# Performance work log

Hardware: AMD Instinct MI355X
Metric: run time of the kernel (lower is better)

## Reference

```python
import jax, jax.numpy as jnp
import numpy as np
from jax import lax

N, T, E = 20000, 64, 640000
H, OUT, HEADS = 128, 64, 3
NEG_SLOPE = 0.2  # GATConv default negative_slope


def setup_inputs() -> dict:
    key = jax.random.key(0)
    ks = jax.random.split(key, 10)
    s = 0.1
    return {
        "node_features": jax.random.normal(ks[0], (N, T), jnp.float32),
        "edge_index": jax.random.randint(ks[1], (2, E), 0, N, dtype=jnp.int32),
        "edge_attributes": jax.random.uniform(ks[2], (E,), jnp.float32),
        "lstm_Wih": jax.random.normal(ks[3], (4 * H, 1), jnp.float32) * s,
        "lstm_Whh": jax.random.normal(ks[4], (4 * H, H), jnp.float32) * s,
        "lstm_bih": jnp.zeros((4 * H,), jnp.float32),
        "lstm_bhh": jnp.zeros((4 * H,), jnp.float32),
        "gcn_W": jax.random.normal(ks[5], (H, H), jnp.float32) * s,
        "gcn_b": jnp.zeros((H,), jnp.float32),
        "gat_W": jax.random.normal(ks[6], (HEADS * OUT, H), jnp.float32) * s,
        "gat_att_src": jax.random.normal(ks[7], (HEADS, OUT), jnp.float32) * s,
        "gat_att_dst": jax.random.normal(ks[8], (HEADS, OUT), jnp.float32) * s,
        "gat_b": jnp.zeros((HEADS * OUT,), jnp.float32),
    }


def _lstm_last(x, Wih, Whh, bih, bhh):
    """x: [N, T, 1] -> last hidden state [N, H] (torch gate order i,f,g,o)."""
    n = x.shape[0]
    h_dim = Whh.shape[1]
    b = bih + bhh

    def step(carry, xt):
        h, c = carry
        g = xt @ Wih.T + h @ Whh.T + b  # [N, 4H]
        i, f, gg, o = jnp.split(g, 4, axis=-1)
        c = jax.nn.sigmoid(f) * c + jax.nn.sigmoid(i) * jnp.tanh(gg)
        h = jax.nn.sigmoid(o) * jnp.tanh(c)
        return (h, c), None

    init = (jnp.zeros((n, h_dim), x.dtype), jnp.zeros((n, h_dim), x.dtype))
    (h, _), _ = lax.scan(step, init, jnp.swapaxes(x, 0, 1))
    return h


def _add_self_loops(row, col, n):
    loop = jnp.arange(n, dtype=row.dtype)
    return jnp.concatenate([row, loop]), jnp.concatenate([col, loop])


def _gcn(x, row, col, edge_weight, W, b):
    """PyG GCNConv: self-loops (weight 1), symmetric normalization, W x + b."""
    n = x.shape[0]
    row, col = _add_self_loops(row, col, n)
    ew = jnp.concatenate([edge_weight, jnp.ones((n,), edge_weight.dtype)])
    x = x @ W.T  # [N, H]
    deg = jax.ops.segment_sum(ew, col, num_segments=n)
    dinv = jnp.where(deg > 0, deg ** -0.5, 0.0)
    norm = dinv[row] * ew * dinv[col]  # [E+N]
    out = jax.ops.segment_sum(x[row] * norm[:, None], col, num_segments=n)
    return out + b


def _gat(x, row, col, W, att_src, att_dst, b):
    """PyG GATConv (concat=True): self-loops, edge softmax over incoming edges."""
    n = x.shape[0]
    heads, c = att_src.shape
    xh = (x @ W.T).reshape(n, heads, c)  # [N, Hd, C]
    a_src = jnp.einsum('nhc,hc->nh', xh, att_src)  # [N, Hd]
    a_dst = jnp.einsum('nhc,hc->nh', xh, att_dst)
    row, col = _add_self_loops(row, col, n)
    alpha = jax.nn.leaky_relu(a_src[row] + a_dst[col], NEG_SLOPE)  # [E', Hd]
    amax = jax.ops.segment_max(alpha, col, num_segments=n)
    alpha = jnp.exp(alpha - amax[col])
    denom = jax.ops.segment_sum(alpha, col, num_segments=n)
    alpha = alpha / denom[col]
    out = jax.ops.segment_sum(xh[row] * alpha[:, :, None], col, num_segments=n)
    return out.reshape(n, heads * c) + b


def reference(node_features, edge_index, edge_attributes,
              lstm_Wih, lstm_Whh, lstm_bih, lstm_bhh,
              gcn_W, gcn_b, gat_W, gat_att_src, gat_att_dst, gat_b):
    x = node_features[:, :, None]  # [N, T, 1]
    x = _lstm_last(x, lstm_Wih, lstm_Whh, lstm_bih, lstm_bhh)  # [N, H]
    x = jax.nn.relu(x)
    row, col = edge_index[0], edge_index[1]
    x = _gcn(x, row, col, edge_attributes, gcn_W, gcn_b)
    x = jax.nn.relu(x)
    x = _gat(x, row, col, gat_W, gat_att_src, gat_att_dst, gat_b)  # [N, Hd*C]
    return jnp.mean(x, axis=0, keepdims=True)  # global_mean_pool, batch=None -> [1, Hd*C]
```

## Files before the change

### kernel.cpp

```cpp
#include <hip/hip_runtime.h>


#define N_NODES 20000
#define T_STEPS 64
#define N_EDGES 640000
#define HDIM    128
#define JOUT    192
#define NEG_SLOPE 0.2f
#define EDGE_CAP 128
#define NBW     16
#define NGRP    5
#define NBB     (NBW * NGRP)
#define BTHR    640
#define NBLK    250
#define GRIDX   256
#define LDS_W     131072
#define LDS_BW    4096
#define LDS_SCR   (NGRP * 4096)
#define LDS_FLG   256
#define LDS_TOTAL (LDS_W + LDS_BW + LDS_SCR + LDS_FLG)

#define L2E  1.4426950408889634f
#define K2E  2.8853900817779268f

typedef _Float16 half8 __attribute__((ext_vector_type(8)));
typedef _Float16 half4v __attribute__((ext_vector_type(4)));
typedef _Float16 half2v __attribute__((ext_vector_type(2)));
typedef float floatx4 __attribute__((ext_vector_type(4)));

__device__ __forceinline__ float lrelu(float x) { return x > 0.f ? x : NEG_SLOPE * x; }

__global__ void pack_whh_kernel(const float* __restrict__ Whh,
                                _Float16* __restrict__ Wpack)
{
  int i = blockIdx.x * 256 + threadIdx.x;
  int tile = i >> 6, lane = i & 63;
  int nt = tile >> 2, kt = tile & 3;
  int row = nt * 16 + (lane & 15);
  int c0  = kt * 32 + (lane >> 4) * 8;
  const float sc = ((row >> 7) == 2) ? K2E : L2E;
  half8 v;
  #pragma unroll
  for (int j = 0; j < 8; ++j)
    v[j] = (_Float16)(Whh[row * 128 + c0 + j] * sc);
  *(half8*)&Wpack[(size_t)i * 8] = v;
}

template <int M>
__global__ void pack_w_kernel(const float* __restrict__ W,
                              _Float16* __restrict__ P)
{
  int i = blockIdx.x * 256 + threadIdx.x;
  int tile = i >> 6, lane = i & 63;
  int mt = tile >> 2, kt = tile & 3;
  int row = mt * 16 + (lane & 15);
  int c0  = kt * 32 + (lane >> 4) * 8;
  half8 v;
  #pragma unroll
  for (int j = 0; j < 8; ++j)
    v[j] = (_Float16)W[row * 128 + c0 + j];
  *(half8*)&P[(size_t)i * 8] = v;
}


#define INITACC(L, acc) do {                                                  \
  _Pragma("unroll") for (int g_ = 0; g_ < 4; ++g_) {                          \
    const float4 p0_ = *(const float4*)&bwRole[g_ * 128 + (L) * 16];          \
    const float4 p1_ = *(const float4*)&bwRole[g_ * 128 + (L) * 16 + 2];      \
    acc[g_][0] = p0_.x + xv * p0_.y;                                          \
    acc[g_][1] = p0_.z + xv * p0_.w;                                          \
    acc[g_][2] = p1_.x + xv * p1_.y;                                          \
    acc[g_][3] = p1_.z + xv * p1_.w;                                          \
  }                                                                           \
} while (0)

#define LDA(buf, L, KT) do {                                                  \
  _Pragma("unroll") for (int g_ = 0; g_ < 4; ++g_)                            \
    buf[g_] = *(const half8*)&WlRole[g_ * 16384 + (L) * 2048 + (KT) * 512];   \
} while (0)

#define MFA(acc, buf, KT) do {                                                \
  _Pragma("unroll") for (int g_ = 0; g_ < 4; ++g_)                            \
    acc[g_] = __builtin_amdgcn_mfma_f32_16x16x32_f16(                         \
        buf[g_], Bf[(KT)], acc[g_], 0, 0, 0);                                 \
} while (0)

#define PHASE4(L, acc) do {                                                   \
  const int cg_ = cgb + (L);                                                  \
  half4v hpack;                                                               \
  _Pragma("unroll") for (int r_ = 0; r_ < 4; ++r_) {                          \
    const float Be = __builtin_amdgcn_exp2f(-acc[0][r_]);                     \
    const float Ae = __builtin_amdgcn_exp2f(-acc[1][r_]);                     \
    const float De = __builtin_amdgcn_exp2f(acc[2][r_]);                      \
    const float Ee = __builtin_amdgcn_exp2f(-acc[3][r_]);                     \
    const float Ap = Ae + 1.f;                                                \
    const float Bp = Be + 1.f;                                                \
    const float Dp = De + 1.f;                                                \
    const float Nn = cst[(L) * 4 + r_] * Bp * Dp + Ap * (De - 1.f);           \
    const float cv = Nn * __builtin_amdgcn_rcpf(Ap * Bp * Dp);                \
    cst[(L) * 4 + r_] = cv;                                                   \
    const float cvc = fminf(fmaxf(cv, -10.f), 10.f);                          \
    const float Fe = __builtin_amdgcn_exp2f(K2E * cvc);                       \
    hpack[r_] = (_Float16)((Fe - 1.f) *                                       \
                __builtin_amdgcn_rcpf((Ee + 1.f) * (Fe + 1.f)));              \
  }                                                                           \
  const int lp_ = nl + 16 * (2 * (cg_ & 1) + wq_hi);                          \
  *(half4v*)&myscr[(cg_ >> 1) * 512 + lp_ * 8 + j0] = hpack;                  \
} while (0)

#define SB __builtin_amdgcn_sched_barrier(0)

#define SIGNAL(arr, val) do {                                                 \
  __threadfence_block();                                                      \
  if (ln == 0) arr[wv] = (val);                                               \
} while (0)
#define WAITGE(arr, val) do {                                                 \
  if (ln == 0) { while (arr[pw] < (val)) __builtin_amdgcn_s_sleep(1); }       \
  __builtin_amdgcn_wave_barrier();                                            \
  __threadfence_block();                                                      \
} while (0)

#define LSTM_STEP(t) do {                                                     \
  WAITGE(flW, (t));                                                           \
  half8 Bf[4];                                                                \
  _Pragma("unroll") for (int kt_ = 0; kt_ < 4; ++kt_)                         \
    Bf[kt_] = *(const half8*)&scrLane[kt_ * 512];                             \
  SIGNAL(flR, (t) + 1);                                                       \
  floatx4 accA[4], accB[4];                                                   \
  half8 Aa[4], Ab[4];                                                         \
                                                                  \
  INITACC(0, accA);                                                           \
  LDA(Aa, 0, 0); LDA(Ab, 0, 1);                                               \
  MFA(accA, Aa, 0); LDA(Aa, 0, 2);                                            \
  MFA(accA, Ab, 1); LDA(Ab, 0, 3);                                            \
  MFA(accA, Aa, 2); MFA(accA, Ab, 3);                                         \
                                                                  \
  INITACC(1, accB); LDA(Aa, 1, 0); LDA(Ab, 1, 1);                             \
  WAITGE(flR, (t) + 1);                                                       \
  SB; PHASE4(0, accA);                                                        \
  MFA(accB, Aa, 0); LDA(Aa, 1, 2);                                            \
  MFA(accB, Ab, 1); LDA(Ab, 1, 3);                                            \
  MFA(accB, Aa, 2); MFA(accB, Ab, 3);                                         \
                                                                  \
  INITACC(2, accA); LDA(Aa, 2, 0); LDA(Ab, 2, 1);                             \
  SB; PHASE4(1, accB);                                                        \
  MFA(accA, Aa, 0); LDA(Aa, 2, 2);                                            \
  MFA(accA, Ab, 1); LDA(Ab, 2, 3);                                            \
  MFA(accA, Aa, 2); MFA(accA, Ab, 3);                                         \
                                                                  \
  INITACC(3, accB); LDA(Aa, 3, 0); LDA(Ab, 3, 1);                             \
  SB; PHASE4(2, accA);                                                        \
  MFA(accB, Aa, 0); LDA(Aa, 3, 2);                                            \
  MFA(accB, Ab, 1); LDA(Ab, 3, 3);                                            \
  MFA(accB, Aa, 2); MFA(accB, Ab, 3);                                         \
  PHASE4(3, accB);                                                            \
  SIGNAL(flW, (t) + 1);                                                       \
} while (0)

__global__ __attribute__((amdgpu_flat_work_group_size(BTHR, BTHR),
                          amdgpu_waves_per_eu(3, 3)))
void lstm_stream_kernel(
    const float* __restrict__ xfeat, const _Float16* __restrict__ Wpack,
    const float* __restrict__ Wih, const float* __restrict__ bih,
    const float* __restrict__ bhh, _Float16* __restrict__ x1,
    const int* __restrict__ ei, const float* __restrict__ ew,
    int* __restrict__ cnt, int2* __restrict__ pairB)
{
  const int tid  = threadIdx.x;

  if (blockIdx.x >= NBLK) {
    const int stride = (GRIDX - NBLK) * BTHR;
    for (int e = (blockIdx.x - NBLK) * BTHR + tid; e < N_EDGES; e += stride) {
      const int r = ei[e];
      const int c = ei[N_EDGES + e];
      const float w = ew[e];
      const int p = atomicAdd(&cnt[c], 1);
      pairB[(size_t)c * EDGE_CAP + p] = make_int2(r, __float_as_int(w));
    }
    return;
  }

  extern __shared__ char dynlds[];
  _Float16* Wl  = (_Float16*)dynlds;
  float2*   bw  = (float2*)(dynlds + LDS_W);
  _Float16* scr = (_Float16*)(dynlds + LDS_W + LDS_BW);
  volatile int* flR = (volatile int*)(dynlds + LDS_W + LDS_BW + LDS_SCR);
  volatile int* flW = flR + 16;

  const int wv   = tid >> 6;
  const int pw   = wv ^ 1;
  const int grp  = wv >> 1;
  const int role = wv & 1;
  const int cgb  = role * 4;
  const int ln   = tid & 63;
  const int nl   = ln & 15;
  const int quad = ln >> 4;
  const int n0   = blockIdx.x * NBB + grp * NBW;

  {
    const float4* src = (const float4*)Wpack;
    float4* dst = (float4*)Wl;
    for (int i = tid; i < LDS_W / 16; i += BTHR) dst[i] = src[i];
  }
  for (int i = tid; i < 512; i += BTHR) {
    const float sc = ((i >> 7) == 2) ? K2E : L2E;
    bw[i] = make_float2((bih[i] + bhh[i]) * sc, Wih[i] * sc);
  }
  {
    float4* z = (float4*)scr;
    for (int i = tid; i < LDS_SCR / 16; i += BTHR)
      z[i] = make_float4(0.f, 0.f, 0.f, 0.f);
  }
  if (tid < 32) { flR[tid] = 0; flW[tid] = 0; }
  __syncthreads();

  _Float16* myscr = scr + grp * 2048;
  const _Float16* WlRole  = Wl + (size_t)cgb * 2048 + (size_t)ln * 8;
  const float2*   bwRole  = bw + cgb * 16 + quad * 4;
  const _Float16* scrLane = myscr + (size_t)ln * 8;
  const float* xrow = xfeat + (size_t)(n0 + nl) * T_STEPS;

  float cst[16];
  #pragma unroll
  for (int i = 0; i < 16; ++i) cst[i] = 0.f;

  const int wq_hi = quad >> 1;
  const int j0    = (quad & 1) * 4;

  float xv = xrow[0];

  #pragma unroll 1
  for (int t = 0; t < T_STEPS; ++t) {
    const float xn = xrow[(t + 1 <= 63) ? (t + 1) : 63];
    LSTM_STEP(t);
    xv = xn;
  }

  #pragma unroll
  for (int k = 0; k < 2; ++k) {
    const int kt = role * 2 + k;
    half8 hf = *(const half8*)&scrLane[kt * 512];
    #pragma unroll
    for (int j = 0; j < 8; ++j)
      hf[j] = (_Float16)fmaxf((float)hf[j], 0.f);
    *(half8*)&x1[(size_t)(n0 + nl) * HDIM + kt * 32 + quad * 8] = hf;
  }
}

template <int J>
__global__ __launch_bounds__(320) void gemm_mfma(
    const _Float16* __restrict__ X, const _Float16* __restrict__ P,
    _Float16* __restrict__ Y)
{
  const int ln = threadIdx.x & 63;
  const int wv = threadIdx.x >> 6;
  const int node = blockIdx.x * 80 + wv * 16 + (ln & 15);
  const int ko = (ln >> 4) * 8;
  half8 Bf[4];
  #pragma unroll
  for (int kt = 0; kt < 4; ++kt)
    Bf[kt] = *(const half8*)&X[(size_t)node * 128 + kt * 32 + ko];
  #pragma unroll
  for (int m = 0; m < J / 16; ++m) {
    floatx4 acc = {0.f, 0.f, 0.f, 0.f};
    #pragma unroll
    for (int kt = 0; kt < 4; ++kt) {
      const half8 Af = *(const half8*)&P[(size_t)((m * 4 + kt) * 64 + ln) * 8];
      acc = __builtin_amdgcn_mfma_f32_16x16x32_f16(Af, Bf[kt], acc, 0, 0, 0);
    }
    half4v o;
    #pragma unroll
    for (int j = 0; j < 4; ++j) o[j] = (_Float16)acc[j];
    *(half4v*)&Y[(size_t)node * J + m * 16 + (ln >> 4) * 4] = o;
  }
}

__global__ __launch_bounds__(320) void gemm_mfma_att(
    const _Float16* __restrict__ X, const _Float16* __restrict__ P,
    const float* __restrict__ att_src, const float* __restrict__ att_dst,
    _Float16* __restrict__ Y, float4* __restrict__ asrc,
    float4* __restrict__ adst)
{
  __shared__ float aS[JOUT], aD[JOUT];
  const int tid = threadIdx.x;
  for (int i = tid; i < JOUT; i += 320) { aS[i] = att_src[i]; aD[i] = att_dst[i]; }
  __syncthreads();
  const int ln = tid & 63;
  const int wv = tid >> 6;
  const int quad = ln >> 4;
  const int node = blockIdx.x * 80 + wv * 16 + (ln & 15);
  half8 Bf[4];
  #pragma unroll
  for (int kt = 0; kt < 4; ++kt)
    Bf[kt] = *(const half8*)&X[(size_t)node * 128 + kt * 32 + quad * 8];
  float sA[3] = {0.f, 0.f, 0.f}, sD[3] = {0.f, 0.f, 0.f};
  #pragma unroll
  for (int m = 0; m < JOUT / 16; ++m) {
    floatx4 acc = {0.f, 0.f, 0.f, 0.f};
    #pragma unroll
    for (int kt = 0; kt < 4; ++kt) {
      const half8 Af = *(const half8*)&P[(size_t)((m * 4 + kt) * 64 + ln) * 8];
      acc = __builtin_amdgcn_mfma_f32_16x16x32_f16(Af, Bf[kt], acc, 0, 0, 0);
    }
    const int h  = m >> 2;
    const int jo = (m & 3) * 16 + quad * 4;
    half4v o;
    #pragma unroll
    for (int j = 0; j < 4; ++j) {
      sA[h] += acc[j] * aS[h * 64 + jo + j];
      sD[h] += acc[j] * aD[h * 64 + jo + j];
      o[j] = (_Float16)acc[j];
    }
    *(half4v*)&Y[(size_t)node * JOUT + m * 16 + quad * 4] = o;
  }
  #pragma unroll
  for (int h = 0; h < 3; ++h) {
    sA[h] += __shfl_xor(sA[h], 16); sA[h] += __shfl_xor(sA[h], 32);
    sD[h] += __shfl_xor(sD[h], 16); sD[h] += __shfl_xor(sD[h], 32);
  }
  if (quad == 0) {
    asrc[node] = make_float4(sA[0], sA[1], sA[2], 0.f);
    adst[node] = make_float4(sD[0], sD[1], sD[2], 0.f);
  }
}

__global__ void zero_kernel(int* __restrict__ cnt, float* __restrict__ accum)
{
  int i = blockIdx.x * 256 + threadIdx.x;
  if (i < N_NODES) cnt[i] = 0;
  if (i < JOUT) accum[i] = 0.f;
}

__global__ __launch_bounds__(256) void degdinv_kernel(
    const int* __restrict__ cnt, const int2* __restrict__ pairB,
    float* __restrict__ dinv)
{
  const int lane = threadIdx.x & 63;
  const int wv = threadIdx.x >> 6;
  const int c = blockIdx.x * 4 + wv;
  const int cc = cnt[c];
  const size_t base = (size_t)c * EDGE_CAP;
  float s = 0.f;
  for (int k = lane; k < cc; k += 64)
    s += __int_as_float(pairB[base + k].y);
  #pragma unroll
  for (int off = 1; off < 64; off <<= 1) s += __shfl_xor(s, off);
  if (lane == 0) dinv[c] = rsqrtf(s + 1.0f);
}

__global__ __launch_bounds__(256) void gcn_agg_kernel(
    const _Float16* __restrict__ y, const float* __restrict__ dinv,
    const int* __restrict__ cnt, const int2* __restrict__ pairB,
    const float* __restrict__ gcn_b, _Float16* __restrict__ x2)
{
  __shared__ float2 stg[4][64];
  const int lane = threadIdx.x & 63;
  const int wv = threadIdx.x >> 6;
  const int c = blockIdx.x * 4 + wv;
  const float dc = dinv[c];
  const half2v* y2 = (const half2v*)y;
  half2v yc = y2[c * 64 + lane];
  float ax = (float)yc[0] * dc * dc, ay = (float)yc[1] * dc * dc;
  const int cc = cnt[c];
  const size_t base = (size_t)c * EDGE_CAP;
  for (int tb = 0; tb < cc; tb += 64) {
    const int nedge = min(64, cc - tb);
    const int k = tb + lane;
    if (k < cc) {
      const int2 pr = pairB[base + k];
      stg[wv][lane] = make_float2(__int_as_float(pr.x),
                                  __int_as_float(pr.y) * dinv[pr.x] * dc);
    }
    __builtin_amdgcn_wave_barrier();
    int i = 0;
    for (; i + 4 <= nedge; i += 4) {
      float2 p0 = stg[wv][i],     p1 = stg[wv][i + 1];
      float2 p2 = stg[wv][i + 2], p3 = stg[wv][i + 3];
      const half2v a0 = y2[(size_t)__float_as_int(p0.x) * 64 + lane];
      const half2v a1 = y2[(size_t)__float_as_int(p1.x) * 64 + lane];
      const half2v a2 = y2[(size_t)__float_as_int(p2.x) * 64 + lane];
      const half2v a3 = y2[(size_t)__float_as_int(p3.x) * 64 + lane];
      ax += (float)a0[0] * p0.y + (float)a1[0] * p1.y +
            (float)a2[0] * p2.y + (float)a3[0] * p3.y;
      ay += (float)a0[1] * p0.y + (float)a1[1] * p1.y +
            (float)a2[1] * p2.y + (float)a3[1] * p3.y;
    }
    for (; i < nedge; ++i) {
      float2 p0 = stg[wv][i];
      const half2v a0 = y2[(size_t)__float_as_int(p0.x) * 64 + lane];
      ax += (float)a0[0] * p0.y; ay += (float)a0[1] * p0.y;
    }
    __builtin_amdgcn_wave_barrier();
  }
  int j0 = lane * 2;
  half2v o;
  o[0] = (_Float16)fmaxf(ax + gcn_b[j0], 0.f);
  o[1] = (_Float16)fmaxf(ay + gcn_b[j0 + 1], 0.f);
  *(half2v*)&x2[c * 128 + j0] = o;
}

__global__ __launch_bounds__(256) void gat_agg_kernel(
    const _Float16* __restrict__ xh, const float4* __restrict__ asrc,
    const float4* __restrict__ adst, const int* __restrict__ cnt,
    const int2* __restrict__ pairB, float* __restrict__ accum)
{
  __shared__ float4 cstg[4][64];
  const int lane = threadIdx.x & 63;
  const int wv = threadIdx.x >> 6;
  const int c = blockIdx.x * 4 + wv;
  const int cc = cnt[c];
  const size_t base = (size_t)c * EDGE_CAP;
  float4 adc = adst[c];
  float4 asc = asrc[c];
  const float se0 = __expf(lrelu(asc.x + adc.x));
  const float se1 = __expf(lrelu(asc.y + adc.y));
  const float se2 = __expf(lrelu(asc.z + adc.z));

  float o0 = se0 * (float)xh[c * JOUT + lane];
  float o1 = se1 * (float)xh[c * JOUT + 64 + lane];
  float o2 = se2 * (float)xh[c * JOUT + 128 + lane];
  float dp0 = 0.f, dp1 = 0.f, dp2 = 0.f;

  for (int tb = 0; tb < cc; tb += 64) {
    const int nedge = min(64, cc - tb);
    const int k = tb + lane;
    if (k < cc) {
      const int s = pairB[base + k].x;
      const float4 av = asrc[s];
      const float a0 = __expf(lrelu(av.x + adc.x));
      const float a1 = __expf(lrelu(av.y + adc.y));
      const float a2 = __expf(lrelu(av.z + adc.z));
      dp0 += a0; dp1 += a1; dp2 += a2;
      cstg[wv][lane] = make_float4(__int_as_float(s), a0, a1, a2);
    }
    __builtin_amdgcn_wave_barrier();
    int i = 0;
    for (; i + 2 <= nedge; i += 2) {
      float4 q0 = cstg[wv][i], q1 = cstg[wv][i + 1];
      const _Float16* r0 = xh + (size_t)__float_as_int(q0.x) * JOUT;
      const _Float16* r1 = xh + (size_t)__float_as_int(q1.x) * JOUT;
      float a0 = (float)r0[lane], b0 = (float)r0[64 + lane], g0 = (float)r0[128 + lane];
      float a1 = (float)r1[lane], b1 = (float)r1[64 + lane], g1 = (float)r1[128 + lane];
      o0 += q0.y * a0 + q1.y * a1;
      o1 += q0.z * b0 + q1.z * b1;
      o2 += q0.w * g0 + q1.w * g1;
    }
    for (; i < nedge; ++i) {
      float4 q0 = cstg[wv][i];
      const _Float16* r0 = xh + (size_t)__float_as_int(q0.x) * JOUT;
      o0 += q0.y * (float)r0[lane];
      o1 += q0.z * (float)r0[64 + lane];
      o2 += q0.w * (float)r0[128 + lane];
    }
    __builtin_amdgcn_wave_barrier();
  }

  #pragma unroll
  for (int off = 1; off < 64; off <<= 1) {
    dp0 += __shfl_xor(dp0, off);
    dp1 += __shfl_xor(dp1, off);
    dp2 += __shfl_xor(dp2, off);
  }
  const float iv0 = 1.f / (dp0 + se0);
  const float iv1 = 1.f / (dp1 + se1);
  const float iv2 = 1.f / (dp2 + se2);
  o0 *= iv0; o1 *= iv1; o2 *= iv2;

  __shared__ float red[4][JOUT];
  red[wv][lane]       = o0;
  red[wv][64 + lane]  = o1;
  red[wv][128 + lane] = o2;
  __syncthreads();
  if (threadIdx.x < JOUT) {
    float sum = red[0][threadIdx.x] + red[1][threadIdx.x] +
                red[2][threadIdx.x] + red[3][threadIdx.x];
    atomicAdd(&accum[threadIdx.x], sum);
  }
}

__global__ void finalize_kernel(const float* __restrict__ accum,
                                const float* __restrict__ gat_b,
                                float* __restrict__ out)
{
  int j = threadIdx.x;
  if (j < JOUT) out[j] = accum[j] * (1.0f / N_NODES) + gat_b[j];
}

extern "C" void kernel_launch(void* const* d_in, const int* in_sizes, int n_in,
                              void* d_out, int out_size, void* d_ws, size_t ws_size,
                              hipStream_t stream)
{
  const float* xfeat = (const float*)d_in[0];
  const int*   eidx  = (const int*)d_in[1];
  const float* eattr = (const float*)d_in[2];
  const float* Wih   = (const float*)d_in[3];
  const float* Whh   = (const float*)d_in[4];
  const float* bihp  = (const float*)d_in[5];
  const float* bhhp  = (const float*)d_in[6];
  const float* gcnW  = (const float*)d_in[7];
  const float* gcnb  = (const float*)d_in[8];
  const float* gatW  = (const float*)d_in[9];
  const float* attS  = (const float*)d_in[10];
  const float* attD  = (const float*)d_in[11];
  const float* gatb  = (const float*)d_in[12];
  float* out = (float*)d_out;

  char* ws = (char*)d_ws;
  size_t off = 0;
  auto alloc = [&](size_t bytes) {
    char* p = ws + off;
    off += (bytes + 255) & ~size_t(255);
    return p;
  };
  _Float16*  x1     = (_Float16*)alloc((size_t)N_NODES * 128 * 2);
  _Float16*  y      = (_Float16*)alloc((size_t)N_NODES * 128 * 2);
  _Float16*  x2     = (_Float16*)alloc((size_t)N_NODES * 128 * 2);
  _Float16*  xh     = (_Float16*)alloc((size_t)N_NODES * 192 * 2);
  float4*    asrc   = (float4*)alloc((size_t)N_NODES * 16);
  float4*    adst   = (float4*)alloc((size_t)N_NODES * 16);
  float*     dinv   = (float*)alloc((size_t)N_NODES * 4);
  int*       cnt    = (int*)alloc((size_t)N_NODES * 4);
  int2*      pairB  = (int2*)alloc((size_t)N_NODES * EDGE_CAP * 8);
  float*     accum  = (float*)alloc(JOUT * 4);
  _Float16*  wpack  = (_Float16*)alloc(131072);
  _Float16*  wpackG = (_Float16*)alloc((size_t)128 * 128 * 2);
  _Float16*  wpackA = (_Float16*)alloc((size_t)192 * 128 * 2);

  hipFuncSetAttribute((const void*)lstm_stream_kernel,
                      hipFuncAttributeMaxDynamicSharedMemorySize, LDS_TOTAL);

  zero_kernel<<<(N_NODES + 255) / 256, 256, 0, stream>>>(cnt, accum);
  pack_whh_kernel<<<32, 256, 0, stream>>>(Whh, wpack);
  pack_w_kernel<128><<<8, 256, 0, stream>>>(gcnW, wpackG);
  pack_w_kernel<192><<<12, 256, 0, stream>>>(gatW, wpackA);
  lstm_stream_kernel<<<GRIDX, BTHR, LDS_TOTAL, stream>>>(
      xfeat, wpack, Wih, bihp, bhhp, x1, eidx, eattr, cnt, pairB);
  degdinv_kernel<<<N_NODES / 4, 256, 0, stream>>>(cnt, pairB, dinv);
  gemm_mfma<128><<<N_NODES / 80, 320, 0, stream>>>(x1, wpackG, y);
  gcn_agg_kernel<<<N_NODES / 4, 256, 0, stream>>>(y, dinv, cnt, pairB, gcnb, x2);
  gemm_mfma_att<<<N_NODES / 80, 320, 0, stream>>>(x2, wpackA, attS, attD,
                                                  xh, asrc, adst);
  gat_agg_kernel<<<N_NODES / 4, 256, 0, stream>>>(xh, asrc, adst, cnt, pairB, accum);
  finalize_kernel<<<1, 256, 0, stream>>>(accum, gatb, out);
}
```

Measured before the change: 594.2 us.

## Reorder GAT mean-pool to sum per-source attention weights, fuse prep kernels

```diff
diff --git a/kernel.cpp b/kernel.cpp
--- a/kernel.cpp
+++ b/kernel.cpp
@@ -30,36 +30,54 @@
 
 __device__ __forceinline__ float lrelu(float x) { return x > 0.f ? x : NEG_SLOPE * x; }
 
-__global__ void pack_whh_kernel(const float* __restrict__ Whh,
-                                _Float16* __restrict__ Wpack)
-{
-  int i = blockIdx.x * 256 + threadIdx.x;
-  int tile = i >> 6, lane = i & 63;
-  int nt = tile >> 2, kt = tile & 3;
-  int row = nt * 16 + (lane & 15);
-  int c0  = kt * 32 + (lane >> 4) * 8;
-  const float sc = ((row >> 7) == 2) ? K2E : L2E;
-  half8 v;
-  #pragma unroll
-  for (int j = 0; j < 8; ++j)
-    v[j] = (_Float16)(Whh[row * 128 + c0 + j] * sc);
-  *(half8*)&Wpack[(size_t)i * 8] = v;
-}
-
-template <int M>
-__global__ void pack_w_kernel(const float* __restrict__ W,
-                              _Float16* __restrict__ P)
-{
-  int i = blockIdx.x * 256 + threadIdx.x;
-  int tile = i >> 6, lane = i & 63;
-  int mt = tile >> 2, kt = tile & 3;
-  int row = mt * 16 + (lane & 15);
-  int c0  = kt * 32 + (lane >> 4) * 8;
-  half8 v;
-  #pragma unroll
-  for (int j = 0; j < 8; ++j)
-    v[j] = (_Float16)W[row * 128 + c0 + j];
-  *(half8*)&P[(size_t)i * 8] = v;
+__global__ __launch_bounds__(256) void prep_kernel(
+    const float* __restrict__ Whh, _Float16* __restrict__ Wpack,
+    const float* __restrict__ gcnW, _Float16* __restrict__ WpackG,
+    const float* __restrict__ gatW, _Float16* __restrict__ WpackA,
+    int* __restrict__ cnt, float* __restrict__ Wgt, float* __restrict__ accum)
+{
+  const int b = blockIdx.x;
+  const int tid = threadIdx.x;
+  if (b < 32) {
+    int i = b * 256 + tid;
+    int tile = i >> 6, lane = i & 63;
+    int nt = tile >> 2, kt = tile & 3;
+    int row = nt * 16 + (lane & 15);
+    int c0  = kt * 32 + (lane >> 4) * 8;
+    const float sc = ((row >> 7) == 2) ? K2E : L2E;
+    half8 v;
+    #pragma unroll
+    for (int j = 0; j < 8; ++j)
+      v[j] = (_Float16)(Whh[row * 128 + c0 + j] * sc);
+    *(half8*)&Wpack[(size_t)i * 8] = v;
+  } else if (b < 40) {
+    int i = (b - 32) * 256 + tid;
+    int tile = i >> 6, lane = i & 63;
+    int mt = tile >> 2, kt = tile & 3;
+    int row = mt * 16 + (lane & 15);
+    int c0  = kt * 32 + (lane >> 4) * 8;
+    half8 v;
+    #pragma unroll
+    for (int j = 0; j < 8; ++j) v[j] = (_Float16)gcnW[row * 128 + c0 + j];
+    *(half8*)&WpackG[(size_t)i * 8] = v;
+  } else if (b < 52) {
+    int i = (b - 40) * 256 + tid;
+    int tile = i >> 6, lane = i & 63;
+    int mt = tile >> 2, kt = tile & 3;
+    int row = mt * 16 + (lane & 15);
+    int c0  = kt * 32 + (lane >> 4) * 8;
+    half8 v;
+    #pragma unroll
+    for (int j = 0; j < 8; ++j) v[j] = (_Float16)gatW[row * 128 + c0 + j];
+    *(half8*)&WpackA[(size_t)i * 8] = v;
+  } else {
+    int i = (b - 52) * 256 + tid;
+    if (i < N_NODES) {
+      cnt[i] = 0;
+      *(float4*)&Wgt[i * 4] = make_float4(0.f, 0.f, 0.f, 0.f);
+    }
+    if (i < JOUT) accum[i] = 0.f;
+  }
 }
 
 
@@ -247,13 +265,25 @@
   }
 }
 
-template <int J>
-__global__ __launch_bounds__(320) void gemm_mfma(
+__global__ __launch_bounds__(320) void gemm128_deg_kernel(
     const _Float16* __restrict__ X, const _Float16* __restrict__ P,
-    _Float16* __restrict__ Y)
+    _Float16* __restrict__ Y, const int* __restrict__ cnt,
+    const int2* __restrict__ pairB, float* __restrict__ dinv)
 {
   const int ln = threadIdx.x & 63;
   const int wv = threadIdx.x >> 6;
+  if (blockIdx.x >= 250) {
+    const int c = (blockIdx.x - 250) * 5 + wv;
+    const int cc = cnt[c];
+    const size_t base = (size_t)c * EDGE_CAP;
+    float s = 0.f;
+    for (int k = ln; k < cc; k += 64)
+      s += __int_as_float(pairB[base + k].y);
+    #pragma unroll
+    for (int off = 1; off < 64; off <<= 1) s += __shfl_xor(s, off);
+    if (ln == 0) dinv[c] = rsqrtf(s + 1.0f);
+    return;
+  }
   const int node = blockIdx.x * 80 + wv * 16 + (ln & 15);
   const int ko = (ln >> 4) * 8;
   half8 Bf[4];
@@ -261,7 +291,7 @@
   for (int kt = 0; kt < 4; ++kt)
     Bf[kt] = *(const half8*)&X[(size_t)node * 128 + kt * 32 + ko];
   #pragma unroll
-  for (int m = 0; m < J / 16; ++m) {
+  for (int m = 0; m < 8; ++m) {
     floatx4 acc = {0.f, 0.f, 0.f, 0.f};
     #pragma unroll
     for (int kt = 0; kt < 4; ++kt) {
@@ -271,7 +301,7 @@
     half4v o;
     #pragma unroll
     for (int j = 0; j < 4; ++j) o[j] = (_Float16)acc[j];
-    *(half4v*)&Y[(size_t)node * J + m * 16 + (ln >> 4) * 4] = o;
+    *(half4v*)&Y[(size_t)node * 128 + m * 16 + (ln >> 4) * 4] = o;
   }
 }
 
@@ -322,30 +352,6 @@
     asrc[node] = make_float4(sA[0], sA[1], sA[2], 0.f);
     adst[node] = make_float4(sD[0], sD[1], sD[2], 0.f);
   }
-}
-
-__global__ void zero_kernel(int* __restrict__ cnt, float* __restrict__ accum)
-{
-  int i = blockIdx.x * 256 + threadIdx.x;
-  if (i < N_NODES) cnt[i] = 0;
-  if (i < JOUT) accum[i] = 0.f;
-}
-
-__global__ __launch_bounds__(256) void degdinv_kernel(
-    const int* __restrict__ cnt, const int2* __restrict__ pairB,
-    float* __restrict__ dinv)
-{
-  const int lane = threadIdx.x & 63;
-  const int wv = threadIdx.x >> 6;
-  const int c = blockIdx.x * 4 + wv;
-  const int cc = cnt[c];
-  const size_t base = (size_t)c * EDGE_CAP;
-  float s = 0.f;
-  for (int k = lane; k < cc; k += 64)
-    s += __int_as_float(pairB[base + k].y);
-  #pragma unroll
-  for (int off = 1; off < 64; off <<= 1) s += __shfl_xor(s, off);
-  if (lane == 0) dinv[c] = rsqrtf(s + 1.0f);
 }
 
 __global__ __launch_bounds__(256) void gcn_agg_kernel(
@@ -399,31 +405,28 @@
   *(half2v*)&x2[c * 128 + j0] = o;
 }
 
-__global__ __launch_bounds__(256) void gat_agg_kernel(
-    const _Float16* __restrict__ xh, const float4* __restrict__ asrc,
-    const float4* __restrict__ adst, const int* __restrict__ cnt,
-    const int2* __restrict__ pairB, float* __restrict__ accum)
-{
-  __shared__ float4 cstg[4][64];
+__global__ __launch_bounds__(256) void gat_weight_kernel(
+    const float4* __restrict__ asrc, const float4* __restrict__ adst,
+    const int* __restrict__ cnt, const int2* __restrict__ pairB,
+    float* __restrict__ W)
+{
   const int lane = threadIdx.x & 63;
   const int wv = threadIdx.x >> 6;
   const int c = blockIdx.x * 4 + wv;
   const int cc = cnt[c];
   const size_t base = (size_t)c * EDGE_CAP;
-  float4 adc = adst[c];
-  float4 asc = asrc[c];
+  const float4 adc = adst[c];
+  const float4 asc = asrc[c];
   const float se0 = __expf(lrelu(asc.x + adc.x));
   const float se1 = __expf(lrelu(asc.y + adc.y));
   const float se2 = __expf(lrelu(asc.z + adc.z));
-
-  float o0 = se0 * (float)xh[c * JOUT + lane];
-  float o1 = se1 * (float)xh[c * JOUT + 64 + lane];
-  float o2 = se2 * (float)xh[c * JOUT + 128 + lane];
   float dp0 = 0.f, dp1 = 0.f, dp2 = 0.f;
-
-  for (int tb = 0; tb < cc; tb += 64) {
-    const int nedge = min(64, cc - tb);
-    const int k = tb + lane;
+  float a0v[2], a1v[2], a2v[2]; int sv[2];
+  #pragma unroll
+  for (int it = 0; it < 2; ++it) {
+    const int k = it * 64 + lane;
+    sv[it] = -1;
+    a0v[it] = 0.f; a1v[it] = 0.f; a2v[it] = 0.f;
     if (k < cc) {
       const int s = pairB[base + k].x;
       const float4 av = asrc[s];
@@ -431,30 +434,9 @@
       const float a1 = __expf(lrelu(av.y + adc.y));
       const float a2 = __expf(lrelu(av.z + adc.z));
       dp0 += a0; dp1 += a1; dp2 += a2;
-      cstg[wv][lane] = make_float4(__int_as_float(s), a0, a1, a2);
-    }
-    __builtin_amdgcn_wave_barrier();
-    int i = 0;
-    for (; i + 2 <= nedge; i += 2) {
-      float4 q0 = cstg[wv][i], q1 = cstg[wv][i + 1];
-      const _Float16* r0 = xh + (size_t)__float_as_int(q0.x) * JOUT;
-      const _Float16* r1 = xh + (size_t)__float_as_int(q1.x) * JOUT;
-      float a0 = (float)r0[lane], b0 = (float)r0[64 + lane], g0 = (float)r0[128 + lane];
-      float a1 = (float)r1[lane], b1 = (float)r1[64 + lane], g1 = (float)r1[128 + lane];
-      o0 += q0.y * a0 + q1.y * a1;
-      o1 += q0.z * b0 + q1.z * b1;
-      o2 += q0.w * g0 + q1.w * g1;
-    }
-    for (; i < nedge; ++i) {
-      float4 q0 = cstg[wv][i];
-      const _Float16* r0 = xh + (size_t)__float_as_int(q0.x) * JOUT;
-      o0 += q0.y * (float)r0[lane];
-      o1 += q0.z * (float)r0[64 + lane];
-      o2 += q0.w * (float)r0[128 + lane];
-    }
-    __builtin_amdgcn_wave_barrier();
-  }
-
+      sv[it] = s; a0v[it] = a0; a1v[it] = a1; a2v[it] = a2;
+    }
+  }
   #pragma unroll
   for (int off = 1; off < 64; off <<= 1) {
     dp0 += __shfl_xor(dp0, off);
@@ -464,18 +446,32 @@
   const float iv0 = 1.f / (dp0 + se0);
   const float iv1 = 1.f / (dp1 + se1);
   const float iv2 = 1.f / (dp2 + se2);
-  o0 *= iv0; o1 *= iv1; o2 *= iv2;
-
-  __shared__ float red[4][JOUT];
-  red[wv][lane]       = o0;
-  red[wv][64 + lane]  = o1;
-  red[wv][128 + lane] = o2;
-  __syncthreads();
-  if (threadIdx.x < JOUT) {
-    float sum = red[0][threadIdx.x] + red[1][threadIdx.x] +
-                red[2][threadIdx.x] + red[3][threadIdx.x];
-    atomicAdd(&accum[threadIdx.x], sum);
-  }
+  if (lane == 0) {
+    atomicAdd(&W[c * 4 + 0], se0 * iv0);
+    atomicAdd(&W[c * 4 + 1], se1 * iv1);
+    atomicAdd(&W[c * 4 + 2], se2 * iv2);
+  }
+  #pragma unroll
+  for (int it = 0; it < 2; ++it) {
+    if (sv[it] >= 0) {
+      atomicAdd(&W[sv[it] * 4 + 0], a0v[it] * iv0);
+      atomicAdd(&W[sv[it] * 4 + 1], a1v[it] * iv1);
+      atomicAdd(&W[sv[it] * 4 + 2], a2v[it] * iv2);
+    }
+  }
+}
+
+__global__ __launch_bounds__(192) void gat_final_kernel(
+    const _Float16* __restrict__ xh, const float* __restrict__ W,
+    float* __restrict__ accum)
+{
+  const int j = threadIdx.x;
+  const int h = j >> 6;
+  float sum = 0.f;
+  const int s0 = blockIdx.x * 80;
+  for (int s = s0; s < s0 + 80; ++s)
+    sum += W[s * 4 + h] * (float)xh[(size_t)s * JOUT + j];
+  atomicAdd(&accum[j], sum);
 }
 
 __global__ void finalize_kernel(const float* __restrict__ accum,
@@ -521,6 +517,7 @@
   float*     dinv   = (float*)alloc((size_t)N_NODES * 4);
   int*       cnt    = (int*)alloc((size_t)N_NODES * 4);
   int2*      pairB  = (int2*)alloc((size_t)N_NODES * EDGE_CAP * 8);
+  float*     Wgt    = (float*)alloc((size_t)N_NODES * 4 * 4);
   float*     accum  = (float*)alloc(JOUT * 4);
   _Float16*  wpack  = (_Float16*)alloc(131072);
   _Float16*  wpackG = (_Float16*)alloc((size_t)128 * 128 * 2);
@@ -529,17 +526,15 @@
   hipFuncSetAttribute((const void*)lstm_stream_kernel,
                       hipFuncAttributeMaxDynamicSharedMemorySize, LDS_TOTAL);
 
-  zero_kernel<<<(N_NODES + 255) / 256, 256, 0, stream>>>(cnt, accum);
-  pack_whh_kernel<<<32, 256, 0, stream>>>(Whh, wpack);
-  pack_w_kernel<128><<<8, 256, 0, stream>>>(gcnW, wpackG);
-  pack_w_kernel<192><<<12, 256, 0, stream>>>(gatW, wpackA);
+  prep_kernel<<<131, 256, 0, stream>>>(Whh, wpack, gcnW, wpackG, gatW, wpackA,
+                                       cnt, Wgt, accum);
   lstm_stream_kernel<<<GRIDX, BTHR, LDS_TOTAL, stream>>>(
       xfeat, wpack, Wih, bihp, bhhp, x1, eidx, eattr, cnt, pairB);
-  degdinv_kernel<<<N_NODES / 4, 256, 0, stream>>>(cnt, pairB, dinv);
-  gemm_mfma<128><<<N_NODES / 80, 320, 0, stream>>>(x1, wpackG, y);
+  gemm128_deg_kernel<<<4250, 320, 0, stream>>>(x1, wpackG, y, cnt, pairB, dinv);
   gcn_agg_kernel<<<N_NODES / 4, 256, 0, stream>>>(y, dinv, cnt, pairB, gcnb, x2);
   gemm_mfma_att<<<N_NODES / 80, 320, 0, stream>>>(x2, wpackA, attS, attD,
                                                   xh, asrc, adst);
-  gat_agg_kernel<<<N_NODES / 4, 256, 0, stream>>>(xh, asrc, adst, cnt, pairB, accum);
+  gat_weight_kernel<<<N_NODES / 4, 256, 0, stream>>>(asrc, adst, cnt, pairB, Wgt);
+  gat_final_kernel<<<N_NODES / 80, 192, 0, stream>>>(xh, Wgt, accum);
   finalize_kernel<<<1, 256, 0, stream>>>(accum, gatb, out);
 }
```

Measured after the change: 571.5 us. 1.04x faster.
